# Performance work log

Measured on AMD Instinct MI355X. Metric: run time of the kernel, lower is better.

## Reference

```python
import jax, jax.numpy as jnp
import numpy as np

EPS = 1e-6
L, H, D, DFF = 4, 6, 6, 64  # n_layers, num_heads(=dim, head_dim=1), d_hid, ffn hidden


def layernorm(x, w, b):
    mu = jnp.mean(x, axis=-1, keepdims=True)
    var = jnp.mean((x - mu) ** 2, axis=-1, keepdims=True)
    return (x - mu) / jnp.sqrt(var + EPS) * w + b


def autocorr(x, qw, qb, kw, kb, vw, vb, l1w, l1b):
    # x: [B,S,H]; head_dim==1 so per-head Linear is scalar w*x+b per head.
    k_in = jnp.concatenate([x[:, :1], x[:, :-1]], axis=1)   # roll right, first row kept
    v_in = jnp.concatenate([x[:, 1:], x[:, -1:]], axis=1)   # roll left, last row kept
    q = x * qw + qb
    k = k_in * kw + kb
    v = v_in * vw + vb
    teo = q * q - k * v                                      # [B,S,H]
    # nn.LayerNorm([1]) over size-1 axis: mean==x, var==0 -> output is bias
    normed = (teo - teo) / jnp.sqrt(EPS) * l1w + l1b
    scores = jax.nn.softmax(normed, axis=1)                  # over seq dim
    return scores * teo


def mha(x, p, li, ai):
    out = autocorr(x, p['qw'][li, ai], p['qb'][li, ai], p['kw'][li, ai],
                   p['kb'][li, ai], p['vw'][li, ai], p['vb'][li, ai],
                   p['ln1_w'][li, ai], p['ln1_b'][li, ai])
    return layernorm(out + x, p['mha_ln_w'][li, ai], p['mha_ln_b'][li, ai])


def setup_inputs() -> dict:
    key = jax.random.key(0)
    ks = jax.random.split(key, 24)
    n = jax.random.normal
    inp = {
        'x_batch': n(ks[0], (128, 4096, 6), jnp.float32),
        'enc_output': n(ks[1], (128, 4096, 6), jnp.float32),
        'dec_ln_w': jnp.ones((D,), jnp.float32),
        'dec_ln_b': jnp.zeros((D,), jnp.float32),
        'qw': n(ks[2], (L, 2, H), jnp.float32),
        'qb': n(ks[3], (L, 2, H), jnp.float32) * 0.1,
        'kw': n(ks[4], (L, 2, H), jnp.float32),
        'kb': n(ks[5], (L, 2, H), jnp.float32) * 0.1,
        'vw': n(ks[6], (L, 2, H), jnp.float32),
        'vb': n(ks[7], (L, 2, H), jnp.float32) * 0.1,
        'ln1_w': jnp.ones((L, 2), jnp.float32),
        'ln1_b': jnp.zeros((L, 2), jnp.float32),
        'mha_ln_w': jnp.ones((L, 2, D), jnp.float32),
        'mha_ln_b': jnp.zeros((L, 2, D), jnp.float32),
        'ffn_w1': n(ks[8], (L, DFF, D), jnp.float32) * (1.0 / np.sqrt(D)),
        'ffn_b1': jnp.zeros((L, DFF), jnp.float32),
        'ffn_w2': n(ks[9], (L, D, DFF), jnp.float32) * (1.0 / np.sqrt(DFF)),
        'ffn_b2': jnp.zeros((L, D), jnp.float32),
        'ffn_ln_w': jnp.ones((L, D), jnp.float32),
        'ffn_ln_b': jnp.zeros((L, D), jnp.float32),
    }
    return inp


def reference(x_batch, enc_output, dec_ln_w, dec_ln_b, qw, qb, kw, kb, vw, vb,
              ln1_w, ln1_b, mha_ln_w, mha_ln_b, ffn_w1, ffn_b1, ffn_w2, ffn_b2,
              ffn_ln_w, ffn_ln_b):
    p = dict(qw=qw, qb=qb, kw=kw, kb=kb, vw=vw, vb=vb, ln1_w=ln1_w, ln1_b=ln1_b,
             mha_ln_w=mha_ln_w, mha_ln_b=mha_ln_b)
    x = layernorm(x_batch, dec_ln_w, dec_ln_b)  # dropout p=0 -> identity
    for li in range(L):
        x = mha(x, p, li, 0)   # self-attention block
        x = mha(x, p, li, 1)   # "enc" attention block (also self, per source)
        h = jax.nn.relu(jnp.einsum('bsd,fd->bsf', x, ffn_w1[li]) + ffn_b1[li])
        y = jnp.einsum('bsf,df->bsd', h, ffn_w2[li]) + ffn_b2[li] + x
        x = layernorm(y, ffn_ln_w[li], ffn_ln_b[li])
    return x
```

## Files before the change

### kernel.cpp

```cpp
#include <hip/hip_runtime.h>

#define S_LEN  4096
#define DM     6
#define NLAYER 4
#define NFF    64
#define HALO   8
#define TPB    256
#define OUT_PER_WAVE 112
#define BLK_X 10

typedef float    vf2 __attribute__((ext_vector_type(2)));
typedef float    vf4 __attribute__((ext_vector_type(4)));
typedef _Float16 vh2 __attribute__((ext_vector_type(2)));
typedef _Float16 vh4 __attribute__((ext_vector_type(4)));

#define W1A_OFF 0
#define W2A_OFF 2048
#define PACK_TOTAL 4096

#define XSZ (128*16)
#define YSTRIDE 130
#define YROWS 6
#define YSZ (YROWS*YSTRIDE*4)
#define WAVE_LDS (XSZ + YSZ)

__device__ __forceinline__ vf2 splat2(float s){ vf2 r; r.x = s; r.y = s; return r; }
__device__ __forceinline__ unsigned pkh(float a, float b){
    return __builtin_bit_cast(unsigned, __builtin_amdgcn_cvt_pkrtz(a, b));
}
__device__ __forceinline__ unsigned pack2(float lo, float hi){
    _Float16 a = (_Float16)lo, b = (_Float16)hi;
    unsigned short ua = __builtin_bit_cast(unsigned short, a);
    unsigned short ub = __builtin_bit_cast(unsigned short, b);
    return (unsigned)ua | ((unsigned)ub << 16);
}

__global__ void prep_frags(const float* __restrict__ w1,
                           const float* __restrict__ w2,
                           unsigned* __restrict__ ws) {
    int i = blockIdx.x * 256 + threadIdx.x;
    if (i >= PACK_TOTAL) return;
    int which = i >> 11;
    int r  = i & 2047;
    int li = r >> 9;
    int q  = r & 511;
    int tile = q >> 7;
    int rem  = q & 127;
    int lane = rem >> 1;
    int dwj  = rem & 1;
    int c = lane & 15, g = lane >> 4;
    float lo = 0.f, hi = 0.f;
    if (which == 0) {
        int f  = tile*16 + c;
        int d0 = g*4 + 2*dwj;
        if (d0   < DM) lo = w1[li*NFF*DM + f*DM + d0];
        if (d0+1 < DM) hi = w1[li*NFF*DM + f*DM + d0+1];
    } else {
        int d = c;
        int f = tile*16 + g*4 + 2*dwj;
        if (d < DM) { lo = w2[li*DM*NFF + d*NFF + f]; hi = w2[li*DM*NFF + d*NFF + f+1]; }
    }
    ws[i] = pack2(lo, hi);
}

__device__ __forceinline__ void ln6v(vf2* v, const float* __restrict__ w,
                                     const float* __restrict__ b) {
    vf2 mu = (((v[0]+v[1])+(v[2]+v[3]))+(v[4]+v[5])) * (1.0f/6.0f);
    vf2 var = splat2(0.0f);
#pragma unroll
    for (int d = 0; d < DM; ++d) { vf2 dd = v[d]-mu; var = __builtin_elementwise_fma(dd, dd, var); }
    vf2 a = var * (1.0f/6.0f) + splat2(1e-6f);
    vf2 r; r.x = rsqrtf(a.x); r.y = rsqrtf(a.y);
#pragma unroll
    for (int d = 0; d < DM; ++d)
        v[d] = __builtin_elementwise_fma((v[d]-mu)*r, splat2(w[d]), splat2(b[d]));
}

__global__ __launch_bounds__(TPB)
void decoder_fused(const float* __restrict__ x_batch,
                   const float* __restrict__ dec_ln_w, const float* __restrict__ dec_ln_b,
                   const float* __restrict__ qw, const float* __restrict__ qb,
                   const float* __restrict__ kw, const float* __restrict__ kb,
                   const float* __restrict__ vw, const float* __restrict__ vb,
                   const float* __restrict__ mha_ln_w, const float* __restrict__ mha_ln_b,
                   const unsigned* __restrict__ wsp,
                   const float* __restrict__ ffn_b1, const float* __restrict__ ffn_b2,
                   const float* __restrict__ ffn_ln_w, const float* __restrict__ ffn_ln_b,
                   float* __restrict__ out) {
    const int lane = threadIdx.x & 63;
    const int wid  = threadIdx.x >> 6;
    const int w    = blockIdx.x * (TPB/64) + wid;
    const int b    = blockIdx.y;
    const int p    = w * OUT_PER_WAVE - HALO + 2*lane;
    const int c    = lane & 15, g = lane >> 4;

    __shared__ __align__(16) char smem[(TPB/64) * WAVE_LDS];
    char* wbase = smem + wid * WAVE_LDS;
    char* Xb = wbase;
    char* Yb = wbase + XSZ;

    vf2 x2[DM];
    if (p >= 0 && p + 1 < S_LEN) {
        const float4* s = reinterpret_cast<const float4*>(x_batch + ((size_t)b*S_LEN + p)*DM);
        float4 a0 = s[0], a1 = s[1], a2 = s[2];
        x2[0].x=a0.x; x2[1].x=a0.y; x2[2].x=a0.z; x2[3].x=a0.w; x2[4].x=a1.x; x2[5].x=a1.y;
        x2[0].y=a1.z; x2[1].y=a1.w; x2[2].y=a2.x; x2[3].y=a2.y; x2[4].y=a2.z; x2[5].y=a2.w;
    } else {
        const int pc = min(max(p, 0), S_LEN-1);
        const float2* s = reinterpret_cast<const float2*>(x_batch + ((size_t)b*S_LEN + pc)*DM);
        float2 a0 = s[0], a1 = s[1], a2 = s[2];
        x2[0] = splat2(a0.x); x2[1] = splat2(a0.y); x2[2] = splat2(a1.x);
        x2[3] = splat2(a1.y); x2[4] = splat2(a2.x); x2[5] = splat2(a2.y);
    }

    ln6v(x2, dec_ln_w, dec_ln_b);

#pragma unroll 1
    for (int li = 0; li < NLAYER; ++li) {
        vh4 w1f[4], w2f[4]; vf4 b1f[4];
#pragma unroll
        for (int mt = 0; mt < 4; ++mt) {
            uint2 u = *((const uint2*)wsp + (li*4 + mt)*64 + lane);
            w1f[mt] = __builtin_bit_cast(vh4, u);
            uint2 v = *((const uint2*)wsp + (W2A_OFF/2) + (li*4 + mt)*64 + lane);
            w2f[mt] = __builtin_bit_cast(vh4, v);
            float4 bb = *reinterpret_cast<const float4*>(ffn_b1 + li*NFF + mt*16 + g*4);
            vf4 bv; bv.x=bb.x; bv.y=bb.y; bv.z=bb.z; bv.w=bb.w;
            b1f[mt] = bv;
        }

#pragma unroll 1
        for (int ai = 0; ai < 2; ++ai) {
            const int base = (li*2 + ai) * DM;
            vf2 xm[DM], xp[DM];
#pragma unroll
            for (int d = 0; d < DM; ++d) {
                float up = __shfl_up (x2[d].y, 1);
                float dn = __shfl_down(x2[d].x, 1);
                xm[d].x = (p <= 0) ? x2[d].x : up;
                xm[d].y = x2[d].x;
                xp[d].x = x2[d].y;
                xp[d].y = (p + 1 >= S_LEN - 1) ? x2[d].y : dn;
            }
#pragma unroll
            for (int d = 0; d < DM; ++d) {
                vf2 q = __builtin_elementwise_fma(x2[d], splat2(qw[base+d]), splat2(qb[base+d]));
                vf2 k = __builtin_elementwise_fma(xm[d], splat2(kw[base+d]), splat2(kb[base+d]));
                vf2 v = __builtin_elementwise_fma(xp[d], splat2(vw[base+d]), splat2(vb[base+d]));
                vf2 teo = __builtin_elementwise_fma(q, q, -(k*v));
                x2[d] = __builtin_elementwise_fma(teo, splat2(1.0f/(float)S_LEN), x2[d]);
            }
            ln6v(x2, mha_ln_w + base, mha_ln_b + base);
        }

        {
            {
                char* r0 = Xb + lane*32;
                *(uint4*)r0      = make_uint4(pkh(x2[0].x,x2[1].x), pkh(x2[2].x,x2[3].x),
                                              pkh(x2[4].x,x2[5].x), 0u);
                *(uint4*)(r0+16) = make_uint4(pkh(x2[0].y,x2[1].y), pkh(x2[2].y,x2[3].y),
                                              pkh(x2[4].y,x2[5].y), 0u);
            }
            vh4 bfrag[8];
#pragma unroll
            for (int t = 0; t < 8; ++t) {
                vh4 v = *(const vh4*)(Xb + (16*t + c)*16 + (g&1)*8);
                if (g >= 2) v = (vh4)(_Float16)0;
                bfrag[t] = v;
            }

#pragma unroll
            for (int t = 0; t < 8; ++t) {
                vh4 hb[4];
#pragma unroll
                for (int ft = 0; ft < 4; ++ft) {
                    vf4 hc = __builtin_amdgcn_mfma_f32_16x16x16f16(w1f[ft], bfrag[t], b1f[ft], 0, 0, 0);
                    uint2 u = make_uint2(pkh(hc.x,hc.y), pkh(hc.z,hc.w));
                    vh4 hraw = __builtin_bit_cast(vh4, u);
                    vh4 z4 = (vh4)(_Float16)0;
                    hb[ft] = __builtin_elementwise_max(hraw, z4);
                }
                vf4 yacc; yacc.x=0.f; yacc.y=0.f; yacc.z=0.f; yacc.w=0.f;
#pragma unroll
                for (int ks = 0; ks < 4; ++ks)
                    yacc = __builtin_amdgcn_mfma_f32_16x16x16f16(w2f[ks], hb[ks], yacc, 0, 0, 0);
                int col = 16*t + c;
                float* yp = (float*)Yb;
                if (lane < 32) {
                    yp[(g*4+0)*YSTRIDE + col] = yacc.x;
                    yp[(g*4+1)*YSTRIDE + col] = yacc.y;
                }
                if (lane < 16) {
                    yp[2*YSTRIDE + col] = yacc.z;
                    yp[3*YSTRIDE + col] = yacc.w;
                }
            }
            const float* b2 = ffn_b2 + li*DM;
#pragma unroll
            for (int d = 0; d < DM; ++d) {
                float2 yv = *(const float2*)((float*)Yb + d*YSTRIDE + 2*lane);
                vf2 t2; t2.x = yv.x; t2.y = yv.y;
                x2[d] = x2[d] + splat2(b2[d]) + t2;
            }
            ln6v(x2, ffn_ln_w + li*DM, ffn_ln_b + li*DM);
        }
    }

    if (lane >= 4 && lane < 60 && p < S_LEN) {
        float4* dst = reinterpret_cast<float4*>(out + ((size_t)b*S_LEN + p)*DM);
        float4 a0, a1, a2;
        a0.x=x2[0].x; a0.y=x2[1].x; a0.z=x2[2].x; a0.w=x2[3].x;
        a1.x=x2[4].x; a1.y=x2[5].x; a1.z=x2[0].y; a1.w=x2[1].y;
        a2.x=x2[2].y; a2.y=x2[3].y; a2.z=x2[4].y; a2.w=x2[5].y;
        dst[0]=a0; dst[1]=a1; dst[2]=a2;
    }
}

extern "C" void kernel_launch(void* const* d_in, const int* in_sizes, int n_in,
                              void* d_out, int out_size, void* d_ws, size_t ws_size,
                              hipStream_t stream) {
    const float* x_batch  = (const float*)d_in[0];
    const float* dec_ln_w = (const float*)d_in[2];
    const float* dec_ln_b = (const float*)d_in[3];
    const float* qw       = (const float*)d_in[4];
    const float* qb       = (const float*)d_in[5];
    const float* kw       = (const float*)d_in[6];
    const float* kb       = (const float*)d_in[7];
    const float* vw       = (const float*)d_in[8];
    const float* vb       = (const float*)d_in[9];
    const float* mha_ln_w = (const float*)d_in[12];
    const float* mha_ln_b = (const float*)d_in[13];
    const float* ffn_w1   = (const float*)d_in[14];
    const float* ffn_b1   = (const float*)d_in[15];
    const float* ffn_w2   = (const float*)d_in[16];
    const float* ffn_b2   = (const float*)d_in[17];
    const float* ffn_ln_w = (const float*)d_in[18];
    const float* ffn_ln_b = (const float*)d_in[19];
    float* out = (float*)d_out;
    unsigned* wsp = (unsigned*)d_ws;

    prep_frags<<<(PACK_TOTAL + 255)/256, 256, 0, stream>>>(ffn_w1, ffn_w2, wsp);

    const int B = in_sizes[0] / (S_LEN * DM);
    dim3 grid(BLK_X, B);
    decoder_fused<<<grid, TPB, 0, stream>>>(
        x_batch, dec_ln_w, dec_ln_b, qw, qb, kw, kb, vw, vb,
        mha_ln_w, mha_ln_b, wsp, ffn_b1, ffn_b2, ffn_ln_w, ffn_ln_b, out);
}
```

Measured before the change: 140.5 us.

## Map one sequence position per lane instead of two, with smaller wave tiles

Each lane now holds a single sequence position instead of a packed pair, so a wave covers 64 positions and outputs 48. The FFN MFMA loop, LDS staging buffers and halo shuffles shrink to match, and launch bounds now request higher occupancy. The aim is to cut register pressure and raise the number of resident waves to hide latency. The cost is a larger halo overlap: a bigger share of the computed positions are redundant, so total work rises. Global loads also narrow from float4 to float2.

```diff
diff --git a/kernel.cpp b/kernel.cpp
--- a/kernel.cpp
+++ b/kernel.cpp
@@ -6,25 +6,22 @@
 #define NFF    64
 #define HALO   8
 #define TPB    256
-#define OUT_PER_WAVE 112
-#define BLK_X 10
-
-typedef float    vf2 __attribute__((ext_vector_type(2)));
+#define OUT_PER_WAVE 48
+#define BLK_X 22
+
 typedef float    vf4 __attribute__((ext_vector_type(4)));
-typedef _Float16 vh2 __attribute__((ext_vector_type(2)));
 typedef _Float16 vh4 __attribute__((ext_vector_type(4)));
 
 #define W1A_OFF 0
 #define W2A_OFF 2048
 #define PACK_TOTAL 4096
 
-#define XSZ (128*16)
-#define YSTRIDE 130
+#define XSZ (64*16)
+#define YSTRIDE 66
 #define YROWS 6
 #define YSZ (YROWS*YSTRIDE*4)
 #define WAVE_LDS (XSZ + YSZ)
 
-__device__ __forceinline__ vf2 splat2(float s){ vf2 r; r.x = s; r.y = s; return r; }
 __device__ __forceinline__ unsigned pkh(float a, float b){
     return __builtin_bit_cast(unsigned, __builtin_amdgcn_cvt_pkrtz(a, b));
 }
@@ -63,20 +60,18 @@
     ws[i] = pack2(lo, hi);
 }
 
-__device__ __forceinline__ void ln6v(vf2* v, const float* __restrict__ w,
-                                     const float* __restrict__ b) {
-    vf2 mu = (((v[0]+v[1])+(v[2]+v[3]))+(v[4]+v[5])) * (1.0f/6.0f);
-    vf2 var = splat2(0.0f);
-#pragma unroll
-    for (int d = 0; d < DM; ++d) { vf2 dd = v[d]-mu; var = __builtin_elementwise_fma(dd, dd, var); }
-    vf2 a = var * (1.0f/6.0f) + splat2(1e-6f);
-    vf2 r; r.x = rsqrtf(a.x); r.y = rsqrtf(a.y);
-#pragma unroll
-    for (int d = 0; d < DM; ++d)
-        v[d] = __builtin_elementwise_fma((v[d]-mu)*r, splat2(w[d]), splat2(b[d]));
-}
-
-__global__ __launch_bounds__(TPB)
+__device__ __forceinline__ void ln6(float* v, const float* __restrict__ w,
+                                    const float* __restrict__ b) {
+    float mu = (((v[0]+v[1])+(v[2]+v[3]))+(v[4]+v[5])) * (1.0f/6.0f);
+    float var = 0.0f;
+#pragma unroll
+    for (int d = 0; d < DM; ++d) { float dd = v[d]-mu; var = fmaf(dd, dd, var); }
+    float r = rsqrtf(fmaf(var, 1.0f/6.0f, 1e-6f));
+#pragma unroll
+    for (int d = 0; d < DM; ++d) v[d] = fmaf((v[d]-mu)*r, w[d], b[d]);
+}
+
+__global__ __launch_bounds__(TPB, 6)
 void decoder_fused(const float* __restrict__ x_batch,
                    const float* __restrict__ dec_ln_w, const float* __restrict__ dec_ln_b,
                    const float* __restrict__ qw, const float* __restrict__ qb,
@@ -90,8 +85,10 @@
     const int lane = threadIdx.x & 63;
     const int wid  = threadIdx.x >> 6;
     const int w    = blockIdx.x * (TPB/64) + wid;
+    if (w * OUT_PER_WAVE - HALO >= S_LEN) return;
     const int b    = blockIdx.y;
-    const int p    = w * OUT_PER_WAVE - HALO + 2*lane;
+    const int p    = w * OUT_PER_WAVE - HALO + lane;
+    const int pc   = min(max(p, 0), S_LEN - 1);
     const int c    = lane & 15, g = lane >> 4;
 
     __shared__ __align__(16) char smem[(TPB/64) * WAVE_LDS];
@@ -99,21 +96,14 @@
     char* Xb = wbase;
     char* Yb = wbase + XSZ;
 
-    vf2 x2[DM];
-    if (p >= 0 && p + 1 < S_LEN) {
-        const float4* s = reinterpret_cast<const float4*>(x_batch + ((size_t)b*S_LEN + p)*DM);
-        float4 a0 = s[0], a1 = s[1], a2 = s[2];
-        x2[0].x=a0.x; x2[1].x=a0.y; x2[2].x=a0.z; x2[3].x=a0.w; x2[4].x=a1.x; x2[5].x=a1.y;
-        x2[0].y=a1.z; x2[1].y=a1.w; x2[2].y=a2.x; x2[3].y=a2.y; x2[4].y=a2.z; x2[5].y=a2.w;
-    } else {
-        const int pc = min(max(p, 0), S_LEN-1);
+    float x[DM];
+    {
         const float2* s = reinterpret_cast<const float2*>(x_batch + ((size_t)b*S_LEN + pc)*DM);
         float2 a0 = s[0], a1 = s[1], a2 = s[2];
-        x2[0] = splat2(a0.x); x2[1] = splat2(a0.y); x2[2] = splat2(a1.x);
-        x2[3] = splat2(a1.y); x2[4] = splat2(a2.x); x2[5] = splat2(a2.y);
-    }
-
-    ln6v(x2, dec_ln_w, dec_ln_b);
+        x[0]=a0.x; x[1]=a0.y; x[2]=a1.x; x[3]=a1.y; x[4]=a2.x; x[5]=a2.y;
+    }
+
+    ln6(x, dec_ln_w, dec_ln_b);
 
 #pragma unroll 1
     for (int li = 0; li < NLAYER; ++li) {
@@ -132,45 +122,38 @@
 #pragma unroll 1
         for (int ai = 0; ai < 2; ++ai) {
             const int base = (li*2 + ai) * DM;
-            vf2 xm[DM], xp[DM];
+            float xm[DM], xp[DM];
 #pragma unroll
             for (int d = 0; d < DM; ++d) {
-                float up = __shfl_up (x2[d].y, 1);
-                float dn = __shfl_down(x2[d].x, 1);
-                xm[d].x = (p <= 0) ? x2[d].x : up;
-                xm[d].y = x2[d].x;
-                xp[d].x = x2[d].y;
-                xp[d].y = (p + 1 >= S_LEN - 1) ? x2[d].y : dn;
+                float up = __shfl_up (x[d], 1);
+                float dn = __shfl_down(x[d], 1);
+                xm[d] = (p <= 0)         ? x[d] : up;
+                xp[d] = (p >= S_LEN - 1) ? x[d] : dn;
             }
 #pragma unroll
             for (int d = 0; d < DM; ++d) {
-                vf2 q = __builtin_elementwise_fma(x2[d], splat2(qw[base+d]), splat2(qb[base+d]));
-                vf2 k = __builtin_elementwise_fma(xm[d], splat2(kw[base+d]), splat2(kb[base+d]));
-                vf2 v = __builtin_elementwise_fma(xp[d], splat2(vw[base+d]), splat2(vb[base+d]));
-                vf2 teo = __builtin_elementwise_fma(q, q, -(k*v));
-                x2[d] = __builtin_elementwise_fma(teo, splat2(1.0f/(float)S_LEN), x2[d]);
-            }
-            ln6v(x2, mha_ln_w + base, mha_ln_b + base);
+                float q = fmaf(x[d],  qw[base+d], qb[base+d]);
+                float k = fmaf(xm[d], kw[base+d], kb[base+d]);
+                float v = fmaf(xp[d], vw[base+d], vb[base+d]);
+                float teo = fmaf(q, q, -(k*v));
+                x[d] = fmaf(teo, 1.0f/(float)S_LEN, x[d]);
+            }
+            ln6(x, mha_ln_w + base, mha_ln_b + base);
         }
 
         {
-            {
-                char* r0 = Xb + lane*32;
-                *(uint4*)r0      = make_uint4(pkh(x2[0].x,x2[1].x), pkh(x2[2].x,x2[3].x),
-                                              pkh(x2[4].x,x2[5].x), 0u);
-                *(uint4*)(r0+16) = make_uint4(pkh(x2[0].y,x2[1].y), pkh(x2[2].y,x2[3].y),
-                                              pkh(x2[4].y,x2[5].y), 0u);
-            }
-            vh4 bfrag[8];
-#pragma unroll
-            for (int t = 0; t < 8; ++t) {
+            *(uint4*)(Xb + lane*16) = make_uint4(pkh(x[0],x[1]), pkh(x[2],x[3]),
+                                                 pkh(x[4],x[5]), 0u);
+            vh4 bfrag[4];
+#pragma unroll
+            for (int t = 0; t < 4; ++t) {
                 vh4 v = *(const vh4*)(Xb + (16*t + c)*16 + (g&1)*8);
                 if (g >= 2) v = (vh4)(_Float16)0;
                 bfrag[t] = v;
             }
 
 #pragma unroll
-            for (int t = 0; t < 8; ++t) {
+            for (int t = 0; t < 4; ++t) {
                 vh4 hb[4];
 #pragma unroll
                 for (int ft = 0; ft < 4; ++ft) {
@@ -197,22 +180,17 @@
             }
             const float* b2 = ffn_b2 + li*DM;
 #pragma unroll
-            for (int d = 0; d < DM; ++d) {
-                float2 yv = *(const float2*)((float*)Yb + d*YSTRIDE + 2*lane);
-                vf2 t2; t2.x = yv.x; t2.y = yv.y;
-                x2[d] = x2[d] + splat2(b2[d]) + t2;
-            }
-            ln6v(x2, ffn_ln_w + li*DM, ffn_ln_b + li*DM);
+            for (int d = 0; d < DM; ++d)
+                x[d] = x[d] + b2[d] + ((float*)Yb)[d*YSTRIDE + lane];
+            ln6(x, ffn_ln_w + li*DM, ffn_ln_b + li*DM);
         }
     }
 
-    if (lane >= 4 && lane < 60 && p < S_LEN) {
-        float4* dst = reinterpret_cast<float4*>(out + ((size_t)b*S_LEN + p)*DM);
-        float4 a0, a1, a2;
-        a0.x=x2[0].x; a0.y=x2[1].x; a0.z=x2[2].x; a0.w=x2[3].x;
-        a1.x=x2[4].x; a1.y=x2[5].x; a1.z=x2[0].y; a1.w=x2[1].y;
-        a2.x=x2[2].y; a2.y=x2[3].y; a2.z=x2[4].y; a2.w=x2[5].y;
-        dst[0]=a0; dst[1]=a1; dst[2]=a2;
+    if (lane >= HALO && lane < 64 - HALO && p < S_LEN) {
+        float2* dst = reinterpret_cast<float2*>(out + ((size_t)b*S_LEN + p)*DM);
+        dst[0] = make_float2(x[0], x[1]);
+        dst[1] = make_float2(x[2], x[3]);
+        dst[2] = make_float2(x[4], x[5]);
     }
 }
 
```

Result: no change. 141.4 us (+0.6%).
